# Performance work log

Measured on AMD Instinct MI355X. Metric: run time of the kernel, lower is better.

Reference implementation:

```python
import jax, jax.numpy as jnp
import numpy as np

ENC_HID = 512
DEC_HID = 512


def setup_inputs() -> dict:
    key = jax.random.key(0)
    k1, k2, k3, k4, k5 = jax.random.split(key, 5)
    hidden = jax.random.normal(k1, (64, DEC_HID), dtype=jnp.float32)
    encoder_outputs = jax.random.normal(k2, (1024, 64, 2 * ENC_HID), dtype=jnp.float32)
    in_dim = 2 * ENC_HID + DEC_HID
    # Linear params (stored as [in, out] for x @ W + b)
    scale = 1.0 / np.sqrt(in_dim)
    W = jax.random.uniform(k3, (in_dim, DEC_HID), dtype=jnp.float32, minval=-scale, maxval=scale)
    b = jax.random.uniform(k4, (DEC_HID,), dtype=jnp.float32, minval=-scale, maxval=scale)
    v = jax.random.uniform(k5, (DEC_HID,), dtype=jnp.float32)  # torch.rand in [0,1)
    return {"hidden": hidden, "encoder_outputs": encoder_outputs, "W": W, "b": b, "v": v}


def reference(hidden, encoder_outputs, W, b, v):
    # hidden: [B, Dd]; encoder_outputs: [S, B, 2*De]
    src_len = encoder_outputs.shape[0]
    enc = jnp.transpose(encoder_outputs, (1, 0, 2))            # [B, S, 2*De]
    hid = jnp.broadcast_to(hidden[:, None, :], (hidden.shape[0], src_len, hidden.shape[1]))  # [B, S, Dd]
    concat = jnp.concatenate([hid, enc], axis=2)               # [B, S, Dd+2*De]
    energy = jnp.tanh(concat @ W + b)                          # [B, S, Dd]
    scores = jnp.einsum("bsd,d->bs", energy, v)                # [B, S]
    return jax.nn.softmax(scores, axis=1)
```

## Files before the change

kernel.cpp:

```cpp
#include <hip/hip_runtime.h>
#include <stdint.h>


typedef float  floatx4 __attribute__((ext_vector_type(4)));
typedef __bf16 bf16x8  __attribute__((ext_vector_type(8)));
typedef short  short8  __attribute__((ext_vector_type(8)));

union bfu { bf16x8 v; short8 s; };

#define LOG2E_X2 2.8853900817779268f
#define SB() __builtin_amdgcn_sched_barrier(0)

#define BAR()                                              \
  do {                                                     \
    asm volatile("s_waitcnt lgkmcnt(0)" ::: "memory");     \
    SB();                                                  \
    __builtin_amdgcn_s_barrier();                          \
    SB();                                                  \
  } while (0)

__device__ __forceinline__ void async_ld16(const void* g, void* l) {
  __builtin_amdgcn_global_load_lds(
      (const __attribute__((address_space(1))) void*)g,
      (__attribute__((address_space(3))) void*)l, 16, 0, 0);
}

__global__ void wt_convert(const float* __restrict__ W, __bf16* __restrict__ Bp) {
  __shared__ float tile[64][65];
  const int kt = blockIdx.x >> 3;
  const int nt = blockIdx.x & 7;
  const int c  = threadIdx.x & 63;
  const int r4 = threadIdx.x >> 6;
  #pragma unroll 4
  for (int i = 0; i < 16; i++) {
    int r = i * 4 + r4;
    tile[r][c] = W[(long)(512 + kt * 64 + r) * 512 + nt * 64 + c];
  }
  __syncthreads();
  const int n_loc = threadIdx.x & 63;
  const int kc4   = threadIdx.x >> 6;
  const int n_g   = nt * 64 + n_loc;
  const int wc    = n_g >> 7;
  const int ct    = (n_g >> 4) & 7;
  const int t     = n_g & 15;
  #pragma unroll
  for (int i = 0; i < 2; i++) {
    int chunk = i * 4 + kc4;
    int k_g   = kt * 64 + chunk * 8;
    int T     = k_g >> 5;
    int q     = (k_g >> 3) & 3;
    union bfu u;
    #pragma unroll
    for (int j = 0; j < 8; j++) u.v[j] = (__bf16)tile[chunk * 8 + j][n_loc];
    long cidx = ((long)(T * 4 + wc) * 8 + ct) * 64 + q * 16 + t;
    *(bf16x8*)(Bp + cidx * 8) = u.v;
  }
}

__global__ void hproj_kernel(const float* __restrict__ hidden,
                             const float* __restrict__ W,
                             const float* __restrict__ bias,
                             float* __restrict__ hproj) {
  const int tid = threadIdx.x;
  const int b_  = blockIdx.x >> 2;
  const int kc  = blockIdx.x & 3;
  __shared__ float hid[128];
  if (tid < 128) hid[tid] = hidden[b_ * 512 + kc * 128 + tid];
  __syncthreads();
  float acc = (kc == 0) ? bias[tid] : 0.f;
  const float* Wp = W + (long)(kc * 128) * 512 + tid;
  #pragma unroll 8
  for (int k = 0; k < 128; k++) acc = fmaf(hid[k], Wp[(long)k * 512], acc);
  atomicAdd(&hproj[b_ * 512 + tid], acc);
}

__global__ __launch_bounds__(256) void gemm_score(
    const float* __restrict__ enc,
    const __bf16* __restrict__ Bp,
    const float* __restrict__ hproj,
    const float* __restrict__ v,
    float* __restrict__ scores)
{
  __shared__ float ldsA[8][2048];
  __shared__ float bscore[64];

  const int tid  = threadIdx.x;
  const int lane = tid & 63;
  const int wc   = tid >> 6;
  const int q    = lane >> 4;
  const int t    = lane & 15;
  const long m0  = (long)blockIdx.x * 64;

  const int r0 = tid >> 3, s0 = tid & 7;
  const int r1 = r0 + 32;
  const float* src0 = enc + (m0 + r0) * 1024 + ((s0 ^ (r0 & 7)) << 2);
  const float* src1 = enc + (m0 + r1) * 1024 + ((s0 ^ (r1 & 7)) << 2);
  const int d0 = tid * 4;
  const int d1 = 1024 + tid * 4;

  const __bf16* bpb = Bp + (long)wc * 4096 + (long)lane * 8;

  if (tid < 64) bscore[tid] = 0.f;

  floatx4 acc[4][8];
  #pragma unroll
  for (int i = 0; i < 4; i++)
    #pragma unroll
    for (int j = 0; j < 8; j++)
      acc[i][j] = (floatx4){0.f, 0.f, 0.f, 0.f};

  short8 bfr[2][8];

  auto stage = [&](int T) {
    float* db = &ldsA[T & 7][0];
    async_ld16(src0 + T * 32, db + d0);
    async_ld16(src1 + T * 32, db + d1);
  };
  auto loadB = [&](int T, int s) {
    #pragma unroll
    for (int ct = 0; ct < 8; ct++) {
      union bfu u;
      u.v = *(const bf16x8*)(bpb + (long)T * 16384 + ct * 512);
      bfr[s][ct] = u.s;
    }
  };
  auto compute = [&](int T, int bs) {
    const float* bb = &ldsA[T & 7][0];
    #pragma unroll
    for (int rt = 0; rt < 4; rt++) {
      const int r = rt * 16 + t;
      floatx4 f0 = *(const floatx4*)(bb + r * 32 + (((2 * q)     ^ (t & 7)) << 2));
      floatx4 f1 = *(const floatx4*)(bb + r * 32 + (((2 * q + 1) ^ (t & 7)) << 2));
      union bfu u;
      #pragma unroll
      for (int j = 0; j < 4; j++) {
        u.v[j]     = (__bf16)f0[j];
        u.v[4 + j] = (__bf16)f1[j];
      }
      #pragma unroll
      for (int ct = 0; ct < 8; ct++)
        acc[rt][ct] = __builtin_amdgcn_mfma_f32_16x16x32_bf16(
            u.s, bfr[bs][ct], acc[rt][ct], 0, 0, 0);
    }
  };

  stage(0); stage(1); stage(2); stage(3); stage(4); stage(5); stage(6);
  loadB(0, 0); loadB(1, 1);
  asm volatile("s_waitcnt vmcnt(16)" ::: "memory");
  SB();
  __builtin_amdgcn_s_barrier();
  SB();

#define PHASE(T)                                           \
  {                                                        \
    if ((T) > 0) BAR();                                    \
    if ((T) < 25) stage((T) + 7);                          \
    compute((T), (T) & 1);                                 \
    if ((T) < 30) loadB((T) + 2, (T) & 1);                 \
  }

  PHASE(0)  PHASE(1)  PHASE(2)  PHASE(3)
  PHASE(4)  PHASE(5)  PHASE(6)  PHASE(7)
  PHASE(8)  PHASE(9)  PHASE(10) PHASE(11)
  PHASE(12) PHASE(13) PHASE(14) PHASE(15)
  PHASE(16) PHASE(17) PHASE(18) PHASE(19)
  PHASE(20) PHASE(21) PHASE(22) PHASE(23)
  PHASE(24) PHASE(25) PHASE(26) PHASE(27)
  PHASE(28) PHASE(29) PHASE(30) PHASE(31)
#undef PHASE

  float vv[8];
  #pragma unroll
  for (int ct = 0; ct < 8; ct++) vv[ct] = v[wc * 128 + ct * 16 + t];

  #pragma unroll
  for (int rt = 0; rt < 4; rt++) {
    #pragma unroll
    for (int r = 0; r < 4; r++) {
      int row = rt * 16 + q * 4 + r;
      const float* hrow = hproj + row * 512 + wc * 128 + t;
      float s = 0.f;
      #pragma unroll
      for (int ct = 0; ct < 8; ct++) {
        float e  = acc[rt][ct][r] + hrow[ct * 16];
        float ex = __builtin_amdgcn_exp2f(e * LOG2E_X2);
        float th = 1.f - 2.f * __builtin_amdgcn_rcpf(ex + 1.f);
        s = fmaf(vv[ct], th, s);
      }
      s += __shfl_xor(s, 1);
      s += __shfl_xor(s, 2);
      s += __shfl_xor(s, 4);
      s += __shfl_xor(s, 8);
      if (t == 0) atomicAdd(&bscore[row], s);
    }
  }
  __syncthreads();
  if (tid < 64) scores[(long)tid * 1024 + blockIdx.x] = bscore[tid];
}

__global__ void softmax_kernel(const float* __restrict__ scores,
                               float* __restrict__ out) {
  const int b_   = blockIdx.x;
  const int tid  = threadIdx.x;
  const int lane = tid & 63;
  const int wv   = tid >> 6;
  __shared__ float redmax[4], redsum[4];

  float x[4];
  #pragma unroll
  for (int i = 0; i < 4; i++) x[i] = scores[b_ * 1024 + i * 256 + tid];
  float mx = fmaxf(fmaxf(x[0], x[1]), fmaxf(x[2], x[3]));
  #pragma unroll
  for (int off = 1; off < 64; off <<= 1) mx = fmaxf(mx, __shfl_xor(mx, off));
  if (lane == 0) redmax[wv] = mx;
  __syncthreads();
  mx = fmaxf(fmaxf(redmax[0], redmax[1]), fmaxf(redmax[2], redmax[3]));

  float e[4], s = 0.f;
  #pragma unroll
  for (int i = 0; i < 4; i++) { e[i] = __expf(x[i] - mx); s += e[i]; }
  #pragma unroll
  for (int off = 1; off < 64; off <<= 1) s += __shfl_xor(s, off);
  if (lane == 0) redsum[wv] = s;
  __syncthreads();
  s = redsum[0] + redsum[1] + redsum[2] + redsum[3];
  float inv = 1.f / s;
  #pragma unroll
  for (int i = 0; i < 4; i++) out[b_ * 1024 + i * 256 + tid] = e[i] * inv;
}

extern "C" void kernel_launch(void* const* d_in, const int* in_sizes, int n_in,
                              void* d_out, int out_size, void* d_ws, size_t ws_size,
                              hipStream_t stream) {
  (void)in_sizes; (void)n_in; (void)out_size; (void)ws_size;
  const float* hidden = (const float*)d_in[0];
  const float* enc    = (const float*)d_in[1];
  const float* W      = (const float*)d_in[2];
  const float* bias   = (const float*)d_in[3];
  const float* v      = (const float*)d_in[4];
  float* out = (float*)d_out;

  char* ws = (char*)d_ws;
  __bf16* Bp    = (__bf16*)ws;
  float*  hproj = (float*)(ws + (1 << 20));
  float*  scores= (float*)(ws + (1 << 20) + (128 << 10));

  hipMemsetAsync(hproj, 0, 64 * 512 * sizeof(float), stream);
  wt_convert<<<128, 256, 0, stream>>>(W, Bp);
  hproj_kernel<<<256, 512, 0, stream>>>(hidden, W, bias, hproj);
  gemm_score<<<1024, 256, 0, stream>>>(enc, Bp, hproj, v, scores);
  softmax_kernel<<<64, 256, 0, stream>>>(scores, out);
}
```

Before: 470.9 us.

## Stage A through registers, convert to bf16 before LDS, double-buffer per 128-K phase

Replaces the async global-to-LDS fp32 staging ring of 8 buffers with register loads of 128 K-columns per phase, converted to bf16 and written to a two-buffer bf16 LDS tile with XOR swizzling. The MFMA loop then reads ready bf16 fragments directly instead of converting fp32 per rt. It also cuts barriers from 32 to 8 and adds launch_bounds(256,2) so two blocks can share a CU thanks to the smaller LDS footprint. The risks are higher register pressure from holding 8 floatx4 of A in flight, and a shallower prefetch distance than the 7-deep async ring.

```diff
diff --git a/kernel.cpp b/kernel.cpp
--- a/kernel.cpp
+++ b/kernel.cpp
@@ -11,19 +11,13 @@
 #define LOG2E_X2 2.8853900817779268f
 #define SB() __builtin_amdgcn_sched_barrier(0)
 
-#define BAR()                                              \
+#define BARX()                                             \
   do {                                                     \
     asm volatile("s_waitcnt lgkmcnt(0)" ::: "memory");     \
     SB();                                                  \
     __builtin_amdgcn_s_barrier();                          \
     SB();                                                  \
   } while (0)
-
-__device__ __forceinline__ void async_ld16(const void* g, void* l) {
-  __builtin_amdgcn_global_load_lds(
-      (const __attribute__((address_space(1))) void*)g,
-      (__attribute__((address_space(3))) void*)l, 16, 0, 0);
-}
 
 __global__ void wt_convert(const float* __restrict__ W, __bf16* __restrict__ Bp) {
   __shared__ float tile[64][65];
@@ -74,14 +68,14 @@
   atomicAdd(&hproj[b_ * 512 + tid], acc);
 }
 
-__global__ __launch_bounds__(256) void gemm_score(
+__global__ __launch_bounds__(256, 2) void gemm_score(
     const float* __restrict__ enc,
     const __bf16* __restrict__ Bp,
     const float* __restrict__ hproj,
     const float* __restrict__ v,
     float* __restrict__ scores)
 {
-  __shared__ float ldsA[8][2048];
+  __shared__ __bf16 ldsA[2][8192];
   __shared__ float bscore[64];
 
   const int tid  = threadIdx.x;
@@ -91,12 +85,13 @@
   const int t    = lane & 15;
   const long m0  = (long)blockIdx.x * 64;
 
-  const int r0 = tid >> 3, s0 = tid & 7;
-  const int r1 = r0 + 32;
-  const float* src0 = enc + (m0 + r0) * 1024 + ((s0 ^ (r0 & 7)) << 2);
-  const float* src1 = enc + (m0 + r1) * 1024 + ((s0 ^ (r1 & 7)) << 2);
-  const int d0 = tid * 4;
-  const int d1 = 1024 + tid * 4;
+  const int sm  = tid & 63;
+  const int h   = tid >> 6;
+  const int sm8 = sm * 8;
+  const float* ap = enc + (m0 + sm) * 1024 + h * 32;
+
+  const __bf16* ar0 = &ldsA[0][q * 512 + ((t * 8) ^ (q * 16))];
+  const __bf16* ar1 = &ldsA[1][q * 512 + ((t * 8) ^ (q * 16))];
 
   const __bf16* bpb = Bp + (long)wc * 4096 + (long)lane * 8;
 
@@ -109,34 +104,41 @@
     for (int j = 0; j < 8; j++)
       acc[i][j] = (floatx4){0.f, 0.f, 0.f, 0.f};
 
-  short8 bfr[2][8];
-
-  auto stage = [&](int T) {
-    float* db = &ldsA[T & 7][0];
-    async_ld16(src0 + T * 32, db + d0);
-    async_ld16(src1 + T * 32, db + d1);
-  };
-  auto loadB = [&](int T, int s) {
+  floatx4 ra[8];
+  short8  bfr[2][8];
+
+  auto issueA = [&](int P) {
+    const float* p = ap + P * 128;
+    #pragma unroll
+    for (int i = 0; i < 8; i++) ra[i] = *(const floatx4*)(p + i * 4);
+  };
+  auto writeA = [&](int b) {
+    __bf16* dst = &ldsA[b][h * 2048];
+    #pragma unroll
+    for (int i2 = 0; i2 < 4; i2++) {
+      union bfu u;
+      #pragma unroll
+      for (int j = 0; j < 4; j++) {
+        u.v[j]     = (__bf16)ra[2 * i2][j];
+        u.v[4 + j] = (__bf16)ra[2 * i2 + 1][j];
+      }
+      *(bf16x8*)(dst + i2 * 512 + (sm8 ^ (i2 * 16))) = u.v;
+    }
+  };
+  auto loadB = [&](int T, int bs) {
     #pragma unroll
     for (int ct = 0; ct < 8; ct++) {
       union bfu u;
       u.v = *(const bf16x8*)(bpb + (long)T * 16384 + ct * 512);
-      bfr[s][ct] = u.s;
-    }
-  };
-  auto compute = [&](int T, int bs) {
-    const float* bb = &ldsA[T & 7][0];
+      bfr[bs][ct] = u.s;
+    }
+  };
+  auto compute = [&](int b, int s, int bs) {
+    const __bf16* base = (b ? ar1 : ar0) + s * 2048;
     #pragma unroll
     for (int rt = 0; rt < 4; rt++) {
-      const int r = rt * 16 + t;
-      floatx4 f0 = *(const floatx4*)(bb + r * 32 + (((2 * q)     ^ (t & 7)) << 2));
-      floatx4 f1 = *(const floatx4*)(bb + r * 32 + (((2 * q + 1) ^ (t & 7)) << 2));
       union bfu u;
-      #pragma unroll
-      for (int j = 0; j < 4; j++) {
-        u.v[j]     = (__bf16)f0[j];
-        u.v[4 + j] = (__bf16)f1[j];
-      }
+      u.v = *(const bf16x8*)(base + rt * 128);
       #pragma unroll
       for (int ct = 0; ct < 8; ct++)
         acc[rt][ct] = __builtin_amdgcn_mfma_f32_16x16x32_bf16(
@@ -144,29 +146,27 @@
     }
   };
 
-  stage(0); stage(1); stage(2); stage(3); stage(4); stage(5); stage(6);
+  issueA(0);
   loadB(0, 0); loadB(1, 1);
-  asm volatile("s_waitcnt vmcnt(16)" ::: "memory");
-  SB();
-  __builtin_amdgcn_s_barrier();
-  SB();
-
-#define PHASE(T)                                           \
+  writeA(0);
+  BARX();
+
+#define PHASE(P)                                           \
   {                                                        \
-    if ((T) > 0) BAR();                                    \
-    if ((T) < 25) stage((T) + 7);                          \
-    compute((T), (T) & 1);                                 \
-    if ((T) < 30) loadB((T) + 2, (T) & 1);                 \
-  }
-
-  PHASE(0)  PHASE(1)  PHASE(2)  PHASE(3)
-  PHASE(4)  PHASE(5)  PHASE(6)  PHASE(7)
-  PHASE(8)  PHASE(9)  PHASE(10) PHASE(11)
-  PHASE(12) PHASE(13) PHASE(14) PHASE(15)
-  PHASE(16) PHASE(17) PHASE(18) PHASE(19)
-  PHASE(20) PHASE(21) PHASE(22) PHASE(23)
-  PHASE(24) PHASE(25) PHASE(26) PHASE(27)
-  PHASE(28) PHASE(29) PHASE(30) PHASE(31)
+    if ((P) < 7) issueA((P) + 1);                          \
+    compute((P) & 1, 0, 0);                                \
+    loadB((P) * 4 + 2, 0);                                 \
+    compute((P) & 1, 1, 1);                                \
+    loadB((P) * 4 + 3, 1);                                 \
+    compute((P) & 1, 2, 0);                                \
+    if ((P) < 7) loadB((P) * 4 + 4, 0);                    \
+    compute((P) & 1, 3, 1);                                \
+    if ((P) < 7) loadB((P) * 4 + 5, 1);                    \
+    if ((P) < 7) { writeA(((P) & 1) ^ 1); BARX(); }        \
+  }
+
+  PHASE(0) PHASE(1) PHASE(2) PHASE(3)
+  PHASE(4) PHASE(5) PHASE(6) PHASE(7)
 #undef PHASE
 
   float vv[8];
```

Measured after the change: 419.5 us. -10.9%, faster.
